# Kernel optimization log

Hardware: AMD Instinct MI355X
Metric: run time of the kernel (lower is better)

The kernel has to match this reference:

```python
import jax, jax.numpy as jnp
import numpy as np

N = 50000      # nodes
K = 15         # k_max candidate neighbors per node
D = 128        # node_dim
H = 64         # hidden_dim
K_MIN = 2.0
K_MAX = 15.0
TAU = 0.5      # edge_tau
LAM = 1.0      # selector_lambda


def setup_inputs() -> dict:
    key = jax.random.key(0)
    ks = jax.random.split(key, 16)
    x = jax.random.normal(ks[0], (N, D), dtype=jnp.float32)
    src = jax.random.randint(ks[1], (N * K,), 0, N)
    dst = jnp.repeat(jnp.arange(N), K)  # edges grouped by dst, as the module requires
    edge_index = jnp.stack([src, dst]).astype(jnp.int64)
    edge_dist = jax.random.uniform(ks[2], (N * K,), dtype=jnp.float32)

    def lin(k, fin, fout):
        return jax.random.normal(k, (fin, fout), dtype=jnp.float32) / np.sqrt(fin)

    EIN = 2 * D + 1  # edge MLP input: [x_dst, x_src, dist]
    return {
        "x": x, "edge_index": edge_index, "edge_dist": edge_dist,
        "ew1": lin(ks[3], EIN, H), "eb1": jnp.zeros((H,), jnp.float32),
        "ew2": lin(ks[4], H, H),   "eb2": jnp.zeros((H,), jnp.float32),
        "ew3": lin(ks[5], H, 1),   "eb3": jnp.zeros((1,), jnp.float32),
        "dw1": lin(ks[6], D + 1, H), "db1": jnp.zeros((H,), jnp.float32),
        "dw2": lin(ks[7], H, H),     "db2": jnp.zeros((H,), jnp.float32),
        "dw3": lin(ks[8], H, 1),     "db3": jnp.zeros((1,), jnp.float32),
    }


def reference(x, edge_index, edge_dist, ew1, eb1, ew2, eb2, ew3, eb3,
              dw1, db1, dw2, db2, dw3, db3):
    src_mat = edge_index[0].reshape(N, K)              # (N, K)
    x_src = x[src_mat]                                 # gather: (N, K, D)
    x_dst = jnp.broadcast_to(x[:, None, :], (N, K, D))
    edge_feat = jnp.concatenate([x_dst, x_src, edge_dist.reshape(N, K, 1)], axis=-1)

    # edge MLP -> logits (eval mode: no gumbel-logistic noise)
    h = jax.nn.relu(edge_feat @ ew1 + eb1)
    h = jax.nn.relu(h @ ew2 + eb2)
    edge_logits = (h @ ew3 + eb3)[..., 0]              # (N, K)
    edge_energy = jax.nn.sigmoid(edge_logits / TAU)

    # degree MLP -> continuous k per node
    degree_hint = edge_energy.sum(axis=1, keepdims=True)
    g = jax.nn.relu(jnp.concatenate([x, degree_hint], axis=1) @ dw1 + db1)
    g = jax.nn.relu(g @ dw2 + db2)
    k_raw = (g @ dw3 + db3)[:, 0]
    k_cont = K_MIN + (K_MAX - K_MIN) * jax.nn.sigmoid(k_raw)  # (N,)

    # per-node descending sort + straight-through top-k gate
    perm = jnp.argsort(-edge_energy, axis=1)
    energy_sorted = jnp.take_along_axis(edge_energy, perm, axis=1)
    ranks = jnp.arange(1, K + 1, dtype=x.dtype)[None, :]
    gate_soft = jax.nn.sigmoid((k_cont[:, None] - ranks) / LAM)
    k_int = jnp.clip(jnp.round(k_cont), K_MIN, K_MAX)
    gate_hard = (ranks <= k_int[:, None]).astype(gate_soft.dtype)
    gate = gate_soft + jax.lax.stop_gradient(gate_hard - gate_soft)

    gated_sorted = energy_sorted * gate
    inv_perm = jnp.argsort(perm, axis=1)               # undo the sort
    edge_gate = jnp.take_along_axis(gate, inv_perm, axis=1)
    edge_weight = jnp.take_along_axis(gated_sorted, inv_perm, axis=1)

    denom = jnp.maximum(edge_weight.sum(axis=1, keepdims=True), 1e-12)
    edge_weight = edge_weight / denom
    return (edge_weight.reshape(-1), edge_gate.reshape(-1),
            edge_energy.reshape(-1), k_cont)
```

## Files before the change

### kernel.cpp

```cpp
#include <hip/hip_runtime.h>
#include <cmath>

#define NN 50000
#define KK 15
#define DD 128
#define HH 64
#define NKE (NN * KK)

__global__ __launch_bounds__(256) void kP(const float* __restrict__ x,
                                          const float* __restrict__ ew1,
                                          const float* __restrict__ dw1,
                                          float* __restrict__ ws) {
    int lane = threadIdx.x & 63;
    int wv = __builtin_amdgcn_readfirstlane((int)(threadIdx.x >> 6));
    int r0 = blockIdx.x * 32 + wv * 8;
    if (r0 >= NN) return;

    const float* W0 = ew1;
    const float* W1 = ew1 + DD * HH;
    const float* W2 = dw1;
    const float* xw = x + (size_t)r0 * DD;

    float a0[8], a1[8], a2[8];
#pragma unroll
    for (int r = 0; r < 8; ++r) { a0[r] = 0.f; a1[r] = 0.f; a2[r] = 0.f; }

#pragma unroll 1
    for (int i4 = 0; i4 < DD / 4; ++i4) {
        float w00 = W0[(i4 * 4 + 0) * HH + lane];
        float w01 = W0[(i4 * 4 + 1) * HH + lane];
        float w02 = W0[(i4 * 4 + 2) * HH + lane];
        float w03 = W0[(i4 * 4 + 3) * HH + lane];
        float w10 = W1[(i4 * 4 + 0) * HH + lane];
        float w11 = W1[(i4 * 4 + 1) * HH + lane];
        float w12 = W1[(i4 * 4 + 2) * HH + lane];
        float w13 = W1[(i4 * 4 + 3) * HH + lane];
        float w20 = W2[(i4 * 4 + 0) * HH + lane];
        float w21 = W2[(i4 * 4 + 1) * HH + lane];
        float w22 = W2[(i4 * 4 + 2) * HH + lane];
        float w23 = W2[(i4 * 4 + 3) * HH + lane];
#pragma unroll
        for (int r = 0; r < 8; ++r) {
            float4 xv = *(const float4*)(xw + r * DD + i4 * 4);
            a0[r] = fmaf(xv.x, w00, a0[r]);
            a0[r] = fmaf(xv.y, w01, a0[r]);
            a0[r] = fmaf(xv.z, w02, a0[r]);
            a0[r] = fmaf(xv.w, w03, a0[r]);
            a1[r] = fmaf(xv.x, w10, a1[r]);
            a1[r] = fmaf(xv.y, w11, a1[r]);
            a1[r] = fmaf(xv.z, w12, a1[r]);
            a1[r] = fmaf(xv.w, w13, a1[r]);
            a2[r] = fmaf(xv.x, w20, a2[r]);
            a2[r] = fmaf(xv.y, w21, a2[r]);
            a2[r] = fmaf(xv.z, w22, a2[r]);
            a2[r] = fmaf(xv.w, w23, a2[r]);
        }
    }
    float* o0 = ws + (size_t)r0 * HH + lane;
    float* o1 = ws + (size_t)NN * HH + (size_t)r0 * HH + lane;
    float* o2 = ws + 2 * (size_t)NN * HH + (size_t)r0 * HH + lane;
#pragma unroll
    for (int r = 0; r < 8; ++r) {
        o0[r * HH] = a0[r];
        o1[r * HH] = a1[r];
        o2[r * HH] = a2[r];
    }
}

__global__ __launch_bounds__(128, 4) void kE(const int* __restrict__ srcIdx,
                                             const float* __restrict__ dist,
                                             const float* __restrict__ ws,
                                             const float* __restrict__ ew1,
                                             const float* __restrict__ eb1,
                                             const float* __restrict__ ew2,
                                             const float* __restrict__ eb2,
                                             const float* __restrict__ ew3,
                                             const float* __restrict__ eb3,
                                             float* __restrict__ energy_out) {
    int e = blockIdx.x * 128 + threadIdx.x;
    if (e >= NKE) return;
    int s = srcIdx[e];
    int d = e / KK;
    float dd = dist[e];
    const float* A = ws + (size_t)d * HH;
    const float* B = ws + (size_t)NN * HH + (size_t)s * HH;
    const float* w1l = ew1 + 2 * DD * HH;

    float acc[HH];
#pragma unroll
    for (int j = 0; j < HH; ++j) acc[j] = 0.f;

    float4 a4 = *(const float4*)A;
    float4 b4 = *(const float4*)B;
#pragma unroll 1
    for (int i4 = 0; i4 < HH / 4; ++i4) {
        float4 a = a4, b = b4;
        int nx = (i4 + 1 < HH / 4) ? (i4 + 1) : i4;
        a4 = *(const float4*)(A + nx * 4);
        b4 = *(const float4*)(B + nx * 4);
        float h[4];
        h[0] = fmaxf(a.x + b.x + dd * w1l[i4 * 4 + 0] + eb1[i4 * 4 + 0], 0.f);
        h[1] = fmaxf(a.y + b.y + dd * w1l[i4 * 4 + 1] + eb1[i4 * 4 + 1], 0.f);
        h[2] = fmaxf(a.z + b.z + dd * w1l[i4 * 4 + 2] + eb1[i4 * 4 + 2], 0.f);
        h[3] = fmaxf(a.w + b.w + dd * w1l[i4 * 4 + 3] + eb1[i4 * 4 + 3], 0.f);
#pragma unroll
        for (int k = 0; k < 4; ++k) {
            const float* wr = ew2 + (i4 * 4 + k) * HH;
#pragma unroll
            for (int j4 = 0; j4 < 16; ++j4) {
                float4 w = *(const float4*)(wr + j4 * 4);
                acc[j4 * 4 + 0] = fmaf(h[k], w.x, acc[j4 * 4 + 0]);
                acc[j4 * 4 + 1] = fmaf(h[k], w.y, acc[j4 * 4 + 1]);
                acc[j4 * 4 + 2] = fmaf(h[k], w.z, acc[j4 * 4 + 2]);
                acc[j4 * 4 + 3] = fmaf(h[k], w.w, acc[j4 * 4 + 3]);
            }
        }
    }
    float lg = eb3[0];
#pragma unroll
    for (int j = 0; j < HH; ++j)
        lg = fmaf(fmaxf(acc[j] + eb2[j], 0.f), ew3[j], lg);
    energy_out[e] = 1.f / (1.f + expf(-2.f * lg));
}

__global__ __launch_bounds__(128, 4) void kF(const float* __restrict__ ws,
                                             const float* __restrict__ dw1,
                                             const float* __restrict__ db1,
                                             const float* __restrict__ dw2,
                                             const float* __restrict__ db2,
                                             const float* __restrict__ dw3,
                                             const float* __restrict__ db3,
                                             float* __restrict__ out) {
    int n = blockIdx.x * 128 + threadIdx.x;
    if (n >= NN) return;
    const float* energy = out + 2 * (size_t)NKE;

    float ev[KK];
    float dh = 0.f;
#pragma unroll
    for (int j = 0; j < KK; ++j) {
        ev[j] = energy[(size_t)n * KK + j];
        dh += ev[j];
    }

    const float* XC = ws + 2 * (size_t)NN * HH + (size_t)n * HH;
    const float* w1l = dw1 + DD * HH;

    float acc[HH];
#pragma unroll
    for (int j = 0; j < HH; ++j) acc[j] = 0.f;

    float4 c4 = *(const float4*)XC;
#pragma unroll 1
    for (int i4 = 0; i4 < HH / 4; ++i4) {
        float4 c = c4;
        int nx = (i4 + 1 < HH / 4) ? (i4 + 1) : i4;
        c4 = *(const float4*)(XC + nx * 4);
        float cv[4] = {c.x, c.y, c.z, c.w};
#pragma unroll
        for (int m = 0; m < 4; ++m) {
            int k = i4 * 4 + m;
            float g = fmaxf(cv[m] + dh * w1l[k] + db1[k], 0.f);
            const float* wr = dw2 + k * HH;
#pragma unroll
            for (int j4 = 0; j4 < 16; ++j4) {
                float4 w = *(const float4*)(wr + j4 * 4);
                acc[j4 * 4 + 0] = fmaf(g, w.x, acc[j4 * 4 + 0]);
                acc[j4 * 4 + 1] = fmaf(g, w.y, acc[j4 * 4 + 1]);
                acc[j4 * 4 + 2] = fmaf(g, w.z, acc[j4 * 4 + 2]);
                acc[j4 * 4 + 3] = fmaf(g, w.w, acc[j4 * 4 + 3]);
            }
        }
    }
    float kraw = db3[0];
#pragma unroll
    for (int j = 0; j < HH; ++j)
        kraw = fmaf(fmaxf(acc[j] + db2[j], 0.f), dw3[j], kraw);

    float kcont = 2.f + 13.f / (1.f + expf(-kraw));
    out[3 * (size_t)NKE + n] = kcont;

    float se[16];
    int si[16];
#pragma unroll
    for (int j = 0; j < KK; ++j) { se[j] = ev[j]; si[j] = j; }
    se[15] = -1.f; si[15] = 15;

#pragma unroll
    for (int p = 1; p < 16; p <<= 1) {
#pragma unroll
        for (int k = p; k >= 1; k >>= 1) {
#pragma unroll
            for (int j = k & (p - 1); j + k < 16; j += 2 * k) {
#pragma unroll
                for (int i = 0; i < k; ++i) {
                    int a = i + j, b = i + j + k;
                    if (b < 16 && (a / (2 * p)) == (b / (2 * p))) {
                        bool sw = (se[b] > se[a]) ||
                                  (se[b] == se[a] && si[b] < si[a]);
                        float ea = sw ? se[b] : se[a];
                        float eb = sw ? se[a] : se[b];
                        int ia = sw ? si[b] : si[a];
                        int ib = sw ? si[a] : si[b];
                        se[a] = ea; se[b] = eb; si[a] = ia; si[b] = ib;
                    }
                }
            }
        }
    }

    float kint = rintf(kcont);
    kint = fminf(fmaxf(kint, 2.f), 15.f);

    float wsrt[KK];
    float denom = 0.f;
#pragma unroll
    for (int r = 0; r < KK; ++r) {
        float sel = ((float)(r + 1) <= kint) ? 1.f : 0.f;
        float wvv = se[r] * sel;
        wsrt[r] = wvv;
        denom += wvv;
    }
    denom = fmaxf(denom, 1e-12f);

#pragma unroll
    for (int r = 0; r < KK; ++r) {
        float sel = ((float)(r + 1) <= kint) ? 1.f : 0.f;
        int j0 = si[r];
        out[(size_t)NKE + (size_t)n * KK + j0] = sel;
        out[(size_t)n * KK + j0] = wsrt[r] / denom;
    }
}

extern "C" void kernel_launch(void* const* d_in, const int* in_sizes, int n_in,
                              void* d_out, int out_size, void* d_ws, size_t ws_size,
                              hipStream_t stream) {
    const float* x   = (const float*)d_in[0];
    const int*   ei  = (const int*)d_in[1];
    const float* ed  = (const float*)d_in[2];
    const float* ew1 = (const float*)d_in[3];
    const float* eb1 = (const float*)d_in[4];
    const float* ew2 = (const float*)d_in[5];
    const float* eb2 = (const float*)d_in[6];
    const float* ew3 = (const float*)d_in[7];
    const float* eb3 = (const float*)d_in[8];
    const float* dw1 = (const float*)d_in[9];
    const float* db1 = (const float*)d_in[10];
    const float* dw2 = (const float*)d_in[11];
    const float* db2 = (const float*)d_in[12];
    const float* dw3 = (const float*)d_in[13];
    const float* db3 = (const float*)d_in[14];
    float* out = (float*)d_out;
    float* ws  = (float*)d_ws;

    hipLaunchKernelGGL(kP, dim3((NN + 31) / 32), dim3(256), 0, stream,
                       x, ew1, dw1, ws);
    hipLaunchKernelGGL(kE, dim3((NKE + 127) / 128), dim3(128), 0, stream,
                       ei, ed, ws, ew1, eb1, ew2, eb2, ew3, eb3,
                       out + 2 * (size_t)NKE);
    hipLaunchKernelGGL(kF, dim3((NN + 127) / 128), dim3(128), 0, stream,
                       ws, dw1, db1, dw2, db2, dw3, db3, out);
}
```

Baseline: 269.3 us.

## Transpose x and compute node projections thread-per-node with uniform weight loads

Adds a transpose kernel that writes x in column-major order, and a new projection kernel in which each thread owns one node and accumulates all 64 outputs. Weight reads are wave-uniform and x reads are coalesced. When the workspace is too small, the old row-tiled projection kernel is kept as a fallback. The edge kernel now prefetches the gathered source row two steps ahead to hide gather latency. The transpose adds an extra launch and a full read and write of x.

```diff
diff --git a/kernel.cpp b/kernel.cpp
--- a/kernel.cpp
+++ b/kernel.cpp
@@ -6,25 +6,94 @@
 #define DD 128
 #define HH 64
 #define NKE (NN * KK)
-
-__global__ __launch_bounds__(256) void kP(const float* __restrict__ x,
-                                          const float* __restrict__ ew1,
-                                          const float* __restrict__ dw1,
-                                          float* __restrict__ ws) {
+#define TOFF ((size_t)DD * NN)
+#define WS_NEED ((TOFF + 3 * (size_t)NN * HH) * 4)
+
+__global__ __launch_bounds__(256) void kT(const float* __restrict__ x,
+                                          float* __restrict__ xT) {
+    __shared__ float s[64][DD + 1];
+    int t = threadIdx.x;
+    int r0 = blockIdx.x * 64;
+#pragma unroll
+    for (int i = 0; i < 8; ++i) {
+        int idx = i * 256 + t;
+        int rr = idx >> 5, cc = idx & 31;
+        if (r0 + rr < NN) {
+            float4 v = *(const float4*)(x + (size_t)(r0 + rr) * DD + cc * 4);
+            s[rr][cc * 4 + 0] = v.x; s[rr][cc * 4 + 1] = v.y;
+            s[rr][cc * 4 + 2] = v.z; s[rr][cc * 4 + 3] = v.w;
+        }
+    }
+    __syncthreads();
+    int lane = t & 63, wq = t >> 6;
+    int n = r0 + lane;
+    if (n >= NN) return;
+#pragma unroll
+    for (int i = 0; i < 32; ++i) {
+        int k = i * 4 + wq;
+        xT[(size_t)k * NN + n] = s[lane][k];
+    }
+}
+
+__global__ __launch_bounds__(128, 4) void kP2(const float* __restrict__ xT,
+                                              const float* __restrict__ ew1,
+                                              const float* __restrict__ dw1,
+                                              float* __restrict__ xabc) {
+    int seg = blockIdx.y;
+    const float* W = (seg == 0) ? ew1 : (seg == 1) ? (ew1 + DD * HH) : dw1;
+    float* o = xabc + (size_t)seg * NN * HH;
+    int n = blockIdx.x * 128 + threadIdx.x;
+    if (n >= NN) return;
+
+    float acc[HH];
+#pragma unroll
+    for (int j = 0; j < HH; ++j) acc[j] = 0.f;
+
+#pragma unroll 1
+    for (int k4 = 0; k4 < DD / 4; ++k4) {
+        float x0 = xT[(size_t)(k4 * 4 + 0) * NN + n];
+        float x1 = xT[(size_t)(k4 * 4 + 1) * NN + n];
+        float x2 = xT[(size_t)(k4 * 4 + 2) * NN + n];
+        float x3 = xT[(size_t)(k4 * 4 + 3) * NN + n];
+        float xv[4] = {x0, x1, x2, x3};
+#pragma unroll
+        for (int m = 0; m < 4; ++m) {
+            const float* wr = W + (k4 * 4 + m) * HH;
+#pragma unroll
+            for (int j4 = 0; j4 < 16; ++j4) {
+                float4 w = *(const float4*)(wr + j4 * 4);
+                acc[j4 * 4 + 0] = fmaf(xv[m], w.x, acc[j4 * 4 + 0]);
+                acc[j4 * 4 + 1] = fmaf(xv[m], w.y, acc[j4 * 4 + 1]);
+                acc[j4 * 4 + 2] = fmaf(xv[m], w.z, acc[j4 * 4 + 2]);
+                acc[j4 * 4 + 3] = fmaf(xv[m], w.w, acc[j4 * 4 + 3]);
+            }
+        }
+    }
+    float* orow = o + (size_t)n * HH;
+#pragma unroll
+    for (int j4 = 0; j4 < 16; ++j4) {
+        float4 v;
+        v.x = acc[j4 * 4 + 0]; v.y = acc[j4 * 4 + 1];
+        v.z = acc[j4 * 4 + 2]; v.w = acc[j4 * 4 + 3];
+        *(float4*)(orow + j4 * 4) = v;
+    }
+}
+
+__global__ __launch_bounds__(256, 4) void kP_fb(const float* __restrict__ x,
+                                                const float* __restrict__ ew1,
+                                                const float* __restrict__ dw1,
+                                                float* __restrict__ xabc) {
     int lane = threadIdx.x & 63;
-    int wv = __builtin_amdgcn_readfirstlane((int)(threadIdx.x >> 6));
+    int wv = threadIdx.x >> 6;
     int r0 = blockIdx.x * 32 + wv * 8;
     if (r0 >= NN) return;
-
     const float* W0 = ew1;
     const float* W1 = ew1 + DD * HH;
     const float* W2 = dw1;
     const float* xw = x + (size_t)r0 * DD;
-
     float a0[8], a1[8], a2[8];
 #pragma unroll
     for (int r = 0; r < 8; ++r) { a0[r] = 0.f; a1[r] = 0.f; a2[r] = 0.f; }
-
 #pragma unroll 1
     for (int i4 = 0; i4 < DD / 4; ++i4) {
         float w00 = W0[(i4 * 4 + 0) * HH + lane];
@@ -42,34 +111,26 @@
 #pragma unroll
         for (int r = 0; r < 8; ++r) {
             float4 xv = *(const float4*)(xw + r * DD + i4 * 4);
-            a0[r] = fmaf(xv.x, w00, a0[r]);
-            a0[r] = fmaf(xv.y, w01, a0[r]);
-            a0[r] = fmaf(xv.z, w02, a0[r]);
-            a0[r] = fmaf(xv.w, w03, a0[r]);
-            a1[r] = fmaf(xv.x, w10, a1[r]);
-            a1[r] = fmaf(xv.y, w11, a1[r]);
-            a1[r] = fmaf(xv.z, w12, a1[r]);
-            a1[r] = fmaf(xv.w, w13, a1[r]);
-            a2[r] = fmaf(xv.x, w20, a2[r]);
-            a2[r] = fmaf(xv.y, w21, a2[r]);
-            a2[r] = fmaf(xv.z, w22, a2[r]);
-            a2[r] = fmaf(xv.w, w23, a2[r]);
-        }
-    }
-    float* o0 = ws + (size_t)r0 * HH + lane;
-    float* o1 = ws + (size_t)NN * HH + (size_t)r0 * HH + lane;
-    float* o2 = ws + 2 * (size_t)NN * HH + (size_t)r0 * HH + lane;
+            a0[r] = fmaf(xv.x, w00, a0[r]); a0[r] = fmaf(xv.y, w01, a0[r]);
+            a0[r] = fmaf(xv.z, w02, a0[r]); a0[r] = fmaf(xv.w, w03, a0[r]);
+            a1[r] = fmaf(xv.x, w10, a1[r]); a1[r] = fmaf(xv.y, w11, a1[r]);
+            a1[r] = fmaf(xv.z, w12, a1[r]); a1[r] = fmaf(xv.w, w13, a1[r]);
+            a2[r] = fmaf(xv.x, w20, a2[r]); a2[r] = fmaf(xv.y, w21, a2[r]);
+            a2[r] = fmaf(xv.z, w22, a2[r]); a2[r] = fmaf(xv.w, w23, a2[r]);
+        }
+    }
+    float* o0 = xabc + (size_t)r0 * HH + lane;
+    float* o1 = xabc + (size_t)NN * HH + (size_t)r0 * HH + lane;
+    float* o2 = xabc + 2 * (size_t)NN * HH + (size_t)r0 * HH + lane;
 #pragma unroll
     for (int r = 0; r < 8; ++r) {
-        o0[r * HH] = a0[r];
-        o1[r * HH] = a1[r];
-        o2[r * HH] = a2[r];
+        o0[r * HH] = a0[r]; o1[r * HH] = a1[r]; o2[r * HH] = a2[r];
     }
 }
 
 __global__ __launch_bounds__(128, 4) void kE(const int* __restrict__ srcIdx,
                                              const float* __restrict__ dist,
-                                             const float* __restrict__ ws,
+                                             const float* __restrict__ xabc,
                                              const float* __restrict__ ew1,
                                              const float* __restrict__ eb1,
                                              const float* __restrict__ ew2,
@@ -82,8 +143,8 @@
     int s = srcIdx[e];
     int d = e / KK;
     float dd = dist[e];
-    const float* A = ws + (size_t)d * HH;
-    const float* B = ws + (size_t)NN * HH + (size_t)s * HH;
+    const float* A = xabc + (size_t)d * HH;
+    const float* B = xabc + (size_t)NN * HH + (size_t)s * HH;
     const float* w1l = ew1 + 2 * DD * HH;
 
     float acc[HH];
@@ -91,13 +152,16 @@
     for (int j = 0; j < HH; ++j) acc[j] = 0.f;
 
     float4 a4 = *(const float4*)A;
-    float4 b4 = *(const float4*)B;
+    float4 bp0 = *(const float4*)B;
+    float4 bp1 = *(const float4*)(B + 4);
 #pragma unroll 1
     for (int i4 = 0; i4 < HH / 4; ++i4) {
-        float4 a = a4, b = b4;
-        int nx = (i4 + 1 < HH / 4) ? (i4 + 1) : i4;
-        a4 = *(const float4*)(A + nx * 4);
-        b4 = *(const float4*)(B + nx * 4);
+        float4 a = a4, b = bp0;
+        int n1 = (i4 + 1 < 16) ? (i4 + 1) : 15;
+        int n2 = (i4 + 2 < 16) ? (i4 + 2) : 15;
+        a4 = *(const float4*)(A + n1 * 4);
+        bp0 = bp1;
+        bp1 = *(const float4*)(B + n2 * 4);
         float h[4];
         h[0] = fmaxf(a.x + b.x + dd * w1l[i4 * 4 + 0] + eb1[i4 * 4 + 0], 0.f);
         h[1] = fmaxf(a.y + b.y + dd * w1l[i4 * 4 + 1] + eb1[i4 * 4 + 1], 0.f);
@@ -123,7 +187,7 @@
     energy_out[e] = 1.f / (1.f + expf(-2.f * lg));
 }
 
-__global__ __launch_bounds__(128, 4) void kF(const float* __restrict__ ws,
+__global__ __launch_bounds__(128, 4) void kF(const float* __restrict__ xabc,
                                              const float* __restrict__ dw1,
                                              const float* __restrict__ db1,
                                              const float* __restrict__ dw2,
@@ -143,7 +207,7 @@
         dh += ev[j];
     }
 
-    const float* XC = ws + 2 * (size_t)NN * HH + (size_t)n * HH;
+    const float* XC = xabc + 2 * (size_t)NN * HH + (size_t)n * HH;
     const float* w1l = dw1 + DD * HH;
 
     float acc[HH];
@@ -154,7 +218,7 @@
 #pragma unroll 1
     for (int i4 = 0; i4 < HH / 4; ++i4) {
         float4 c = c4;
-        int nx = (i4 + 1 < HH / 4) ? (i4 + 1) : i4;
+        int nx = (i4 + 1 < 16) ? (i4 + 1) : 15;
         c4 = *(const float4*)(XC + nx * 4);
         float cv[4] = {c.x, c.y, c.z, c.w};
 #pragma unroll
@@ -253,11 +317,20 @@
     float* out = (float*)d_out;
     float* ws  = (float*)d_ws;
 
-    hipLaunchKernelGGL(kP, dim3((NN + 31) / 32), dim3(256), 0, stream,
-                       x, ew1, dw1, ws);
+    bool big = (ws_size >= WS_NEED);
+    float* xabc = big ? (ws + TOFF) : ws;
+
+    if (big) {
+        hipLaunchKernelGGL(kT, dim3((NN + 63) / 64), dim3(256), 0, stream, x, ws);
+        hipLaunchKernelGGL(kP2, dim3((NN + 127) / 128, 3), dim3(128), 0, stream,
+                           ws, ew1, dw1, xabc);
+    } else {
+        hipLaunchKernelGGL(kP_fb, dim3((NN + 31) / 32), dim3(256), 0, stream,
+                           x, ew1, dw1, xabc);
+    }
     hipLaunchKernelGGL(kE, dim3((NKE + 127) / 128), dim3(128), 0, stream,
-                       ei, ed, ws, ew1, eb1, ew2, eb2, ew3, eb3,
+                       ei, ed, xabc, ew1, eb1, ew2, eb2, ew3, eb3,
                        out + 2 * (size_t)NKE);
     hipLaunchKernelGGL(kF, dim3((NN + 127) / 128), dim3(128), 0, stream,
-                       ws, dw1, db1, dw2, db2, dw3, db3, out);
-}
+                       xabc, dw1, db1, dw2, db2, dw3, db3, out);
+}
```

Result: slower. 326.9 us (+21.4%).
